# Kernel optimization log

Hardware: AMD Instinct MI355X
Metric: run time of the kernel (lower is better)

The kernel has to match this reference:

```python
import jax, jax.numpy as jnp
import numpy as np

B, L, D, CH, H = 16384, 50, 20, 16, 6


def setup_inputs() -> dict:
    key = jax.random.key(0)
    ks = jax.random.split(key, 18)
    s = 0.1
    return {
        "x": jax.random.normal(ks[0], (B, L, D), jnp.float32),
        "we_w": jax.random.normal(ks[1], (CH, D), jnp.float32) * s,
        "we_b": jax.random.normal(ks[2], (CH,), jnp.float32) * s,
        "attn_w": jax.random.normal(ks[3], (CH, CH), jnp.float32) * s,
        "attn_b": jax.random.normal(ks[4], (CH,), jnp.float32) * s,
        "conv1_w": jax.random.normal(ks[5], (CH, CH, 1), jnp.float32) * s,
        "conv1_b": jax.random.normal(ks[6], (CH,), jnp.float32) * s,
        "conv2_w": jax.random.normal(ks[7], (CH, CH, 3), jnp.float32) * s,
        "conv2_b": jax.random.normal(ks[8], (CH,), jnp.float32) * s,
        "conv3_w": jax.random.normal(ks[9], (CH, CH, 5), jnp.float32) * s,
        "conv3_b": jax.random.normal(ks[10], (CH,), jnp.float32) * s,
        "gru_wih": jax.random.normal(ks[11], (3 * H, CH), jnp.float32) * s,
        "gru_whh": jax.random.normal(ks[12], (3 * H, H), jnp.float32) * s,
        "gru_bih": jax.random.normal(ks[13], (3 * H,), jnp.float32) * s,
        "gru_bhh": jax.random.normal(ks[14], (3 * H,), jnp.float32) * s,
        "fc3_w": jax.random.normal(ks[15], (2, 3 * CH + H), jnp.float32) * s,
        "fc3_b": jax.random.normal(ks[16], (2,), jnp.float32) * s,
        "batchsize": B,
    }


def _conv1d(x, w, b, pad):
    # x: [B, C, L], w: [O, I, K] -> [B, O, L]
    y = jax.lax.conv_general_dilated(x, w, (1,), [(pad, pad)],
                                     dimension_numbers=("NCH", "OIH", "NCH"))
    return y + b[None, :, None]


def _gru(xg, wih, whh, bih, bhh):
    # xg: [B, L, CH] -> outputs [B, L, H] (PyTorch GRU equations, h0=0)
    gi = jnp.einsum("blc,gc->blg", xg, wih) + bih  # [B, L, 3H]
    gi_t = jnp.swapaxes(gi, 0, 1)                  # [L, B, 3H]
    h0 = jnp.zeros((xg.shape[0], H), xg.dtype)

    def step(h, gi_step):
        gh = h @ whh.T + bhh
        i_r, i_z, i_n = jnp.split(gi_step, 3, axis=-1)
        h_r, h_z, h_n = jnp.split(gh, 3, axis=-1)
        r = jax.nn.sigmoid(i_r + h_r)
        z = jax.nn.sigmoid(i_z + h_z)
        n = jnp.tanh(i_n + r * h_n)
        h_new = (1.0 - z) * n + z * h
        return h_new, h_new

    _, outs = jax.lax.scan(step, h0, gi_t)
    return jnp.swapaxes(outs, 0, 1)  # [B, L, H]


def reference(x, we_w, we_b, attn_w, attn_b, conv1_w, conv1_b, conv2_w, conv2_b,
              conv3_w, conv3_b, gru_wih, gru_whh, gru_bih, gru_bhh, fc3_w, fc3_b,
              batchsize):
    b = batchsize
    xe = x @ we_w.T + we_b                 # [B, L, CH]
    xr = xe.reshape(b, CH, L)              # RESHAPE (not transpose), as in torch

    lrelu = lambda v: jnp.where(v > 0, v, 0.1 * v)
    x1 = lrelu(_conv1d(xr, conv1_w, conv1_b, 0))
    x2 = lrelu(_conv1d(xr, conv2_w, conv2_b, 1))
    x3 = lrelu(_conv1d(xr, conv3_w, conv3_b, 2))

    xg = xr.reshape(b, L, CH)              # == xe
    x4 = _gru(xg, gru_wih, gru_whh, gru_bih, gru_bhh)  # [B, L, H]

    # dotproduct1: note x4.reshape([B,H,L]) is a reshape, NOT a transpose
    scores = jnp.matmul(x4, x4.reshape(b, H, L)) / H   # [B, L, L]
    alphas = jax.nn.softmax(scores, axis=1)            # softmax over dim=1 as in torch
    y = jnp.matmul(alphas, x4).reshape(b, H, L)        # [B, H, L]
    x_gru = jnp.sum(y, axis=2)                         # [B, H]

    # vectorized per-timestep attention loop: x[:, :, i] over i -> swapaxes
    xt = jnp.swapaxes(xr, 1, 2)                        # [B, L, CH]
    attn = jnp.tanh(xt @ attn_w.T + attn_b)            # [B, L, CH]
    attn1 = jnp.concatenate([attn, attn, attn], axis=2).reshape(b, 3 * CH, L)

    x_cat = jnp.concatenate([x1, x2, x3], axis=1)      # [B, 3CH, L]
    x_cnn = jnp.sum(x_cat * attn1, axis=2)             # [B, 3CH]

    feat = jnp.concatenate([x_cnn, x_gru], axis=1)     # [B, 3CH+H]
    return feat @ fc3_w.T + fc3_b                      # [B, 2]
```

## Files before the change

kernel.cpp:

```cpp
#include <hip/hip_runtime.h>

#define BATCH 16384
#define LSEQ  50
#define DIN   20
#define CHN   16
#define HID   6

__device__ __forceinline__ float frcp(float x){ return __builtin_amdgcn_rcpf(x); }
__device__ __forceinline__ float fsig(float x){ return frcp(1.0f + __expf(-x)); }
__device__ __forceinline__ float ftanh(float x){ float t = __expf(2.0f*x); return (t - 1.0f) * frcp(t + 1.0f); }
__device__ __forceinline__ float lrelu(float v){ return v > 0.0f ? v : 0.1f*v; }

constexpr int SLAB = 2560;

__global__ __launch_bounds__(256, 4) void fused_kernel(
    const float* __restrict__ x,
    const float* __restrict__ we_w, const float* __restrict__ we_b,
    const float* __restrict__ attn_w, const float* __restrict__ attn_b,
    const float* __restrict__ c1w, const float* __restrict__ c1b,
    const float* __restrict__ c2w, const float* __restrict__ c2b,
    const float* __restrict__ c3w, const float* __restrict__ c3b,
    const float* __restrict__ wih, const float* __restrict__ whh,
    const float* __restrict__ bih, const float* __restrict__ bhh,
    const float* __restrict__ fc3w, const float* __restrict__ fc3b,
    float* __restrict__ out)
{
  __shared__ __align__(16) float smem[4 * SLAB];
  const int tid  = threadIdx.x;
  const int wave = tid >> 6;
  const int lane = tid & 63;
  const int b    = blockIdx.x * 4 + wave;

  float* S    = smem + wave * SLAB;
  float* sXE  = S;
  float* sY   = S + 400;
  float* R1   = S + 800;
  float* sX4  = S + 1800;
  float* sX4P = S + 2104;
  float* sFE  = S + 2504;

  const float* xb = x + (size_t)b * (LSEQ * DIN);

  if (lane < LSEQ) {
    float xv[DIN];
    const float4* xr = (const float4*)(xb + lane * DIN);
    #pragma unroll
    for (int q = 0; q < 5; ++q) {
      float4 v = xr[q];
      xv[4*q] = v.x; xv[4*q+1] = v.y; xv[4*q+2] = v.z; xv[4*q+3] = v.w;
    }
    float xe[CHN];
    #pragma unroll
    for (int c = 0; c < CHN; ++c) {
      float a = we_b[c];
      #pragma unroll
      for (int d = 0; d < DIN; ++d) a = fmaf(xv[d], we_w[c * DIN + d], a);
      xe[c] = a;
    }
    float4* xd = (float4*)(sXE + lane * CHN);
    xd[0] = make_float4(xe[0], xe[1], xe[2], xe[3]);
    xd[1] = make_float4(xe[4], xe[5], xe[6], xe[7]);
    xd[2] = make_float4(xe[8], xe[9], xe[10], xe[11]);
    xd[3] = make_float4(xe[12], xe[13], xe[14], xe[15]);
    float gi[18];
    #pragma unroll
    for (int g = 0; g < 18; ++g) {
      float a = bih[g];
      #pragma unroll
      for (int cc = 0; cc < CHN; ++cc) a = fmaf(xe[cc], wih[g * CHN + cc], a);
      gi[g] = a;
    }
    float4* gd = (float4*)(R1 + lane * 20);
    gd[0] = make_float4(gi[0], gi[1], gi[2], gi[3]);
    gd[1] = make_float4(gi[4], gi[5], gi[6], gi[7]);
    gd[2] = make_float4(gi[8], gi[9], gi[10], gi[11]);
    gd[3] = make_float4(gi[12], gi[13], gi[14], gi[15]);
    *(float2*)(R1 + lane * 20 + 16) = make_float2(gi[16], gi[17]);
  }
  __syncthreads();

  {
    const int g18 = (lane < 18) ? lane : 0;
    float wh[HID];
    #pragma unroll
    for (int k = 0; k < HID; ++k) wh[k] = whh[g18 * HID + k];
    const float bh = bhh[g18];
    const int m6 = lane % 6;
    float hh[HID];
    #pragma unroll
    for (int k = 0; k < HID; ++k) hh[k] = 0.0f;
    float hm = 0.0f;
    for (int l = 0; l < LSEQ; ++l) {
      float gh = bh;
      #pragma unroll
      for (int k = 0; k < HID; ++k) gh = fmaf(wh[k], hh[k], gh);
      float ghr = __shfl(gh, m6);
      float ghz = __shfl(gh, m6 + 6);
      float ghn = __shfl(gh, m6 + 12);
      const float* gl = R1 + l * 20;
      float r  = fsig(gl[m6] + ghr);
      float z  = fsig(gl[m6 + 6] + ghz);
      float n  = ftanh(gl[m6 + 12] + r * ghn);
      float hn = fmaf(z, hm - n, n);
      hm = hn;
      #pragma unroll
      for (int k = 0; k < HID; ++k) hh[k] = __shfl(hn, k);
      if (lane < HID) { sX4[l * HID + lane] = hn; sX4P[l * 8 + lane] = hn; }
    }
  }
  __syncthreads();

  if (lane < LSEQ) {
    float a[CHN];
    #pragma unroll
    for (int cc = 0; cc < CHN; ++cc) a[cc] = sXE[cc * LSEQ + lane];
    float o[CHN];
    #pragma unroll
    for (int c = 0; c < CHN; ++c) {
      float acc = attn_b[c];
      #pragma unroll
      for (int cc = 0; cc < CHN; ++cc) acc = fmaf(a[cc], attn_w[c * CHN + cc], acc);
      o[c] = ftanh(acc);
    }
    float4* ad = (float4*)(R1 + lane * CHN);
    ad[0] = make_float4(o[0], o[1], o[2], o[3]);
    ad[1] = make_float4(o[4], o[5], o[6], o[7]);
    ad[2] = make_float4(o[8], o[9], o[10], o[11]);
    ad[3] = make_float4(o[12], o[13], o[14], o[15]);
  }
  __syncthreads();

  {
    float* sAT = R1;
    const int o = lane & 15;
    const int seg = lane >> 4;
    const int L0 = (seg < 2) ? seg * 13 : 26 + (seg - 2) * 12;
    const int NL = (seg < 2) ? 13 : 12;
    int mcl[17];
    #pragma unroll
    for (int mm = 0; mm < 17; ++mm) {
      int m = L0 - 2 + mm;
      mcl[mm] = min(max(m, 0), LSEQ - 1);
    }
    float z1[13], z2[13], z3[13];
    #pragma unroll
    for (int u = 0; u < 13; ++u) { z1[u] = 0.0f; z2[u] = 0.0f; z3[u] = 0.0f; }
    for (int i = 0; i < CHN; ++i) {
      const float w1 = c1w[o * CHN + i];
      float w2a[3], w3a[5];
      #pragma unroll
      for (int t = 0; t < 3; ++t) w2a[t] = c2w[(o * CHN + i) * 3 + t];
      #pragma unroll
      for (int t = 0; t < 5; ++t) w3a[t] = c3w[(o * CHN + i) * 5 + t];
      const float* xrow = sXE + i * LSEQ;
      float xv[17];
      #pragma unroll
      for (int mm = 0; mm < 17; ++mm) {
        float v = xrow[mcl[mm]];
        if (mm < 2 || mm >= 14) {
          int m = L0 - 2 + mm;
          v = (m == mcl[mm]) ? v : 0.0f;
        }
        xv[mm] = v;
      }
      #pragma unroll
      for (int u = 0; u < 13; ++u) {
        z1[u] = fmaf(w1, xv[u + 2], z1[u]);
        z2[u] = fmaf(w2a[0], xv[u + 1], z2[u]);
        z2[u] = fmaf(w2a[1], xv[u + 2], z2[u]);
        z2[u] = fmaf(w2a[2], xv[u + 3], z2[u]);
        z3[u] = fmaf(w3a[0], xv[u],     z3[u]);
        z3[u] = fmaf(w3a[1], xv[u + 1], z3[u]);
        z3[u] = fmaf(w3a[2], xv[u + 2], z3[u]);
        z3[u] = fmaf(w3a[3], xv[u + 3], z3[u]);
        z3[u] = fmaf(w3a[4], xv[u + 4], z3[u]);
      }
    }
    const float b1v = c1b[o], b2v = c2b[o], b3v = c3b[o];
    float a1 = 0.0f, a2 = 0.0f, a3 = 0.0f;
    #pragma unroll
    for (int u = 0; u < 13; ++u) {
      if (u < NL) {
        int l = L0 + u;
        float v1 = lrelu(z1[u] + b1v);
        float v2 = lrelu(z2[u] + b2v);
        float v3 = lrelu(z3[u] + b3v);
        int f1 = o * LSEQ + l;
        int f2 = (CHN + o) * LSEQ + l;
        int f3 = (2 * CHN + o) * LSEQ + l;
        a1 += v1 * sAT[(f1 / 48) * CHN + ((f1 % 48) & 15)];
        a2 += v2 * sAT[(f2 / 48) * CHN + ((f2 % 48) & 15)];
        a3 += v3 * sAT[(f3 / 48) * CHN + ((f3 % 48) & 15)];
      }
    }
    a1 += __shfl_xor(a1, 16); a1 += __shfl_xor(a1, 32);
    a2 += __shfl_xor(a2, 16); a2 += __shfl_xor(a2, 32);
    a3 += __shfl_xor(a3, 16); a3 += __shfl_xor(a3, 32);
    if (lane < CHN) { sFE[o] = a1; sFE[CHN + o] = a2; sFE[2 * CHN + o] = a3; }
  }
  __syncthreads();

  float* sC = R1;
  if (lane < LSEQ) {
    float colj[HID];
    #pragma unroll
    for (int h = 0; h < HID; ++h) colj[h] = sX4[h * LSEQ + lane];
    *(float4*)(sC + lane * 16)     = make_float4(colj[0], colj[1], colj[2], colj[3]);
    *(float2*)(sC + lane * 16 + 4) = make_float2(colj[4], colj[5]);
    float zs = 0.0f;
    for (int i = 0; i < LSEQ; ++i) {
      const float4 r0 = *(const float4*)(sX4P + i * 8);
      const float2 r1 = *(const float2*)(sX4P + i * 8 + 4);
      float s = r0.x * colj[0];
      s = fmaf(r0.y, colj[1], s); s = fmaf(r0.z, colj[2], s);
      s = fmaf(r0.w, colj[3], s); s = fmaf(r1.x, colj[4], s);
      s = fmaf(r1.y, colj[5], s);
      zs += __expf(s * (1.0f / 6.0f));
    }
    const float zi = frcp(zs);
    const float4 q0 = *(const float4*)(sX4P + lane * 8);
    const float2 q1 = *(const float2*)(sX4P + lane * 8 + 4);
    *(float4*)(sC + lane * 16 + 8)  = make_float4(zi*q0.x, zi*q0.y, zi*q0.z, zi*q0.w);
    *(float2*)(sC + lane * 16 + 12) = make_float2(zi*q1.x, zi*q1.y);
  }
  __syncthreads();

  if (lane < LSEQ) {
    float rowi[HID];
    {
      const float4 q0 = *(const float4*)(sX4P + lane * 8);
      const float2 q1 = *(const float2*)(sX4P + lane * 8 + 4);
      rowi[0] = q0.x; rowi[1] = q0.y; rowi[2] = q0.z;
      rowi[3] = q0.w; rowi[4] = q1.x; rowi[5] = q1.y;
    }
    float ya[HID];
    #pragma unroll
    for (int h = 0; h < HID; ++h) ya[h] = 0.0f;
    for (int j = 0; j < LSEQ; ++j) {
      const float4 t0 = *(const float4*)(sC + j * 16);
      const float2 t1 = *(const float2*)(sC + j * 16 + 4);
      float s = rowi[0] * t0.x;
      s = fmaf(rowi[1], t0.y, s); s = fmaf(rowi[2], t0.z, s);
      s = fmaf(rowi[3], t0.w, s); s = fmaf(rowi[4], t1.x, s);
      s = fmaf(rowi[5], t1.y, s);
      const float e = __expf(s * (1.0f / 6.0f));
      const float4 w0 = *(const float4*)(sC + j * 16 + 8);
      const float2 w1 = *(const float2*)(sC + j * 16 + 12);
      ya[0] = fmaf(e, w0.x, ya[0]);
      ya[1] = fmaf(e, w0.y, ya[1]);
      ya[2] = fmaf(e, w0.z, ya[2]);
      ya[3] = fmaf(e, w0.w, ya[3]);
      ya[4] = fmaf(e, w1.x, ya[4]);
      ya[5] = fmaf(e, w1.y, ya[5]);
    }
    *(float2*)(sY + lane * 6)     = make_float2(ya[0], ya[1]);
    *(float2*)(sY + lane * 6 + 2) = make_float2(ya[2], ya[3]);
    *(float2*)(sY + lane * 6 + 4) = make_float2(ya[4], ya[5]);
  }
  __syncthreads();

  if (lane < HID) {
    float s = 0.0f;
    for (int m = 0; m < LSEQ; ++m) s += sY[lane * LSEQ + m];
    sFE[48 + lane] = s;
  }
  __syncthreads();

  if (lane < 2) {
    float acc = fc3b[lane];
    const float* wr = fc3w + lane * 54;
    #pragma unroll
    for (int k = 0; k < 54; ++k) acc = fmaf(wr[k], sFE[k], acc);
    out[(size_t)b * 2 + lane] = acc;
  }
}

extern "C" void kernel_launch(void* const* d_in, const int* in_sizes, int n_in,
                              void* d_out, int out_size, void* d_ws, size_t ws_size,
                              hipStream_t stream) {
  (void)in_sizes; (void)n_in; (void)d_ws; (void)ws_size; (void)out_size;
  fused_kernel<<<BATCH / 4, 256, 0, stream>>>(
      (const float*)d_in[0],
      (const float*)d_in[1],  (const float*)d_in[2],
      (const float*)d_in[3],  (const float*)d_in[4],
      (const float*)d_in[5],  (const float*)d_in[6],
      (const float*)d_in[7],  (const float*)d_in[8],
      (const float*)d_in[9],  (const float*)d_in[10],
      (const float*)d_in[11], (const float*)d_in[12],
      (const float*)d_in[13], (const float*)d_in[14],
      (const float*)d_in[15], (const float*)d_in[16],
      (float*)d_out);
}
```

Baseline: 309.8 us.

## Split fused kernel into embed, per-thread GRU, and tail kernels via workspace

Splits the single fused kernel into three launches. An embedding/input-gate kernel writes xe and gi to global workspace. A GRU kernel then runs one batch element per thread, removing the per-step cross-lane shuffles and the 18-of-64 lane utilisation of the old recurrence. A tail kernel reloads xe and x4 to do the attention, convolutions and dot-product attention. This costs extra global-memory traffic (about 137 MB written and read back) and two extra launches, and it falls back to the fused kernel when the workspace is too small.

```diff
diff --git a/kernel.cpp b/kernel.cpp
--- a/kernel.cpp
+++ b/kernel.cpp
@@ -11,8 +11,333 @@
 __device__ __forceinline__ float ftanh(float x){ float t = __expf(2.0f*x); return (t - 1.0f) * frcp(t + 1.0f); }
 __device__ __forceinline__ float lrelu(float v){ return v > 0.0f ? v : 0.1f*v; }
 
+__global__ __launch_bounds__(256) void k_embed(
+    const float* __restrict__ x,
+    const float* __restrict__ we_w, const float* __restrict__ we_b,
+    const float* __restrict__ wih,  const float* __restrict__ bih,
+    float* __restrict__ xeg, float* __restrict__ gig)
+{
+  const size_t r = (size_t)blockIdx.x * 256 + threadIdx.x;
+  float xv[DIN];
+  const float4* xr = (const float4*)(x + r * DIN);
+  #pragma unroll
+  for (int q = 0; q < 5; ++q) {
+    float4 v = xr[q];
+    xv[4*q] = v.x; xv[4*q+1] = v.y; xv[4*q+2] = v.z; xv[4*q+3] = v.w;
+  }
+  float xe[CHN];
+  #pragma unroll
+  for (int c = 0; c < CHN; ++c) {
+    float a = we_b[c];
+    #pragma unroll
+    for (int d = 0; d < DIN; ++d) a = fmaf(xv[d], we_w[c * DIN + d], a);
+    xe[c] = a;
+  }
+  float4* xo = (float4*)(xeg + r * CHN);
+  xo[0] = make_float4(xe[0],  xe[1],  xe[2],  xe[3]);
+  xo[1] = make_float4(xe[4],  xe[5],  xe[6],  xe[7]);
+  xo[2] = make_float4(xe[8],  xe[9],  xe[10], xe[11]);
+  xo[3] = make_float4(xe[12], xe[13], xe[14], xe[15]);
+  float gi[18];
+  #pragma unroll
+  for (int g = 0; g < 18; ++g) {
+    float a = bih[g];
+    #pragma unroll
+    for (int c = 0; c < CHN; ++c) a = fmaf(xe[c], wih[g * CHN + c], a);
+    gi[g] = a;
+  }
+  float* go = gig + r * 20;
+  ((float4*)go)[0] = make_float4(gi[0],  gi[1],  gi[2],  gi[3]);
+  ((float4*)go)[1] = make_float4(gi[4],  gi[5],  gi[6],  gi[7]);
+  ((float4*)go)[2] = make_float4(gi[8],  gi[9],  gi[10], gi[11]);
+  ((float4*)go)[3] = make_float4(gi[12], gi[13], gi[14], gi[15]);
+  *(float2*)(go + 16) = make_float2(gi[16], gi[17]);
+}
+
+__global__ __launch_bounds__(64) void k_gru(
+    const float* __restrict__ gig,
+    const float* __restrict__ whh, const float* __restrict__ bhh,
+    float* __restrict__ x4g)
+{
+  const int b = blockIdx.x * 64 + threadIdx.x;
+  float wh[18][HID];
+  #pragma unroll
+  for (int g = 0; g < 18; ++g)
+    #pragma unroll
+    for (int k = 0; k < HID; ++k) wh[g][k] = whh[g * HID + k];
+  float bh[18];
+  #pragma unroll
+  for (int g = 0; g < 18; ++g) bh[g] = bhh[g];
+
+  const float* gp = gig + (size_t)b * (LSEQ * 20);
+  float* op = x4g + (size_t)b * (LSEQ * HID);
+
+  float h[HID];
+  #pragma unroll
+  for (int k = 0; k < HID; ++k) h[k] = 0.0f;
+
+  float cur[18];
+  {
+    const float4* q = (const float4*)gp;
+    float4 a0 = q[0], a1 = q[1], a2 = q[2], a3 = q[3];
+    float2 a4 = *(const float2*)(gp + 16);
+    cur[0]=a0.x; cur[1]=a0.y; cur[2]=a0.z; cur[3]=a0.w;
+    cur[4]=a1.x; cur[5]=a1.y; cur[6]=a1.z; cur[7]=a1.w;
+    cur[8]=a2.x; cur[9]=a2.y; cur[10]=a2.z; cur[11]=a2.w;
+    cur[12]=a3.x; cur[13]=a3.y; cur[14]=a3.z; cur[15]=a3.w;
+    cur[16]=a4.x; cur[17]=a4.y;
+  }
+
+  for (int l = 0; l < LSEQ; ++l) {
+    float nxt[18];
+    if (l < LSEQ - 1) {
+      const float* np = gp + (l + 1) * 20;
+      const float4* q = (const float4*)np;
+      float4 a0 = q[0], a1 = q[1], a2 = q[2], a3 = q[3];
+      float2 a4 = *(const float2*)(np + 16);
+      nxt[0]=a0.x; nxt[1]=a0.y; nxt[2]=a0.z; nxt[3]=a0.w;
+      nxt[4]=a1.x; nxt[5]=a1.y; nxt[6]=a1.z; nxt[7]=a1.w;
+      nxt[8]=a2.x; nxt[9]=a2.y; nxt[10]=a2.z; nxt[11]=a2.w;
+      nxt[12]=a3.x; nxt[13]=a3.y; nxt[14]=a3.z; nxt[15]=a3.w;
+      nxt[16]=a4.x; nxt[17]=a4.y;
+    }
+    float gh[18];
+    #pragma unroll
+    for (int g = 0; g < 18; ++g) {
+      float a = bh[g];
+      #pragma unroll
+      for (int k = 0; k < HID; ++k) a = fmaf(wh[g][k], h[k], a);
+      gh[g] = a;
+    }
+    float r6[HID], z6[HID];
+    #pragma unroll
+    for (int m = 0; m < HID; ++m) r6[m] = fsig(cur[m] + gh[m]);
+    #pragma unroll
+    for (int m = 0; m < HID; ++m) z6[m] = fsig(cur[6 + m] + gh[6 + m]);
+    #pragma unroll
+    for (int m = 0; m < HID; ++m) {
+      float n = ftanh(fmaf(r6[m], gh[12 + m], cur[12 + m]));
+      h[m] = fmaf(z6[m], h[m] - n, n);
+    }
+    *(float2*)(op + l * HID)     = make_float2(h[0], h[1]);
+    *(float2*)(op + l * HID + 2) = make_float2(h[2], h[3]);
+    *(float2*)(op + l * HID + 4) = make_float2(h[4], h[5]);
+    #pragma unroll
+    for (int g = 0; g < 18; ++g) cur[g] = nxt[g];
+  }
+}
+
+constexpr int SLAB3 = 2368;
+
+__global__ __launch_bounds__(256, 4) void k_tail(
+    const float* __restrict__ xeg, const float* __restrict__ x4g,
+    const float* __restrict__ attn_w, const float* __restrict__ attn_b,
+    const float* __restrict__ c1w, const float* __restrict__ c1b,
+    const float* __restrict__ c2w, const float* __restrict__ c2b,
+    const float* __restrict__ c3w, const float* __restrict__ c3b,
+    const float* __restrict__ fc3w, const float* __restrict__ fc3b,
+    float* __restrict__ out)
+{
+  __shared__ __align__(16) float smem[4 * SLAB3];
+  const int tid  = threadIdx.x;
+  const int wave = tid >> 6;
+  const int lane = tid & 63;
+  const int b    = blockIdx.x * 4 + wave;
+
+  float* S    = smem + wave * SLAB3;
+  float* sXE  = S;
+  float* sY   = S + 400;
+  float* R1   = S + 800;
+  float* sX4  = S + 1600;
+  float* sX4P = S + 1904;
+  float* sFE  = S + 2304;
+
+  {
+    const float4* xs = (const float4*)(xeg + (size_t)b * 800);
+    float4* xd = (float4*)sXE;
+    #pragma unroll
+    for (int q = 0; q < 3; ++q) xd[lane + 64 * q] = xs[lane + 64 * q];
+    if (lane < 8) xd[lane + 192] = xs[lane + 192];
+    const float4* hs = (const float4*)(x4g + (size_t)b * 300);
+    float4* hd = (float4*)sX4;
+    hd[lane < 64 ? lane : 0] = hs[lane < 64 ? lane : 0];
+    if (lane < 11) hd[lane + 64] = hs[lane + 64];
+  }
+  __syncthreads();
+  if (lane < LSEQ) {
+    float2 a = *(float2*)(sX4 + lane * 6);
+    float2 c = *(float2*)(sX4 + lane * 6 + 2);
+    float2 d = *(float2*)(sX4 + lane * 6 + 4);
+    *(float2*)(sX4P + lane * 8)     = a;
+    *(float2*)(sX4P + lane * 8 + 2) = c;
+    *(float2*)(sX4P + lane * 8 + 4) = d;
+  }
+
+  if (lane < LSEQ) {
+    float a[CHN];
+    #pragma unroll
+    for (int cc = 0; cc < CHN; ++cc) a[cc] = sXE[cc * LSEQ + lane];
+    float o[CHN];
+    #pragma unroll
+    for (int c = 0; c < CHN; ++c) {
+      float acc = attn_b[c];
+      #pragma unroll
+      for (int cc = 0; cc < CHN; ++cc) acc = fmaf(a[cc], attn_w[c * CHN + cc], acc);
+      o[c] = ftanh(acc);
+    }
+    float4* ad = (float4*)(R1 + lane * CHN);
+    ad[0] = make_float4(o[0],  o[1],  o[2],  o[3]);
+    ad[1] = make_float4(o[4],  o[5],  o[6],  o[7]);
+    ad[2] = make_float4(o[8],  o[9],  o[10], o[11]);
+    ad[3] = make_float4(o[12], o[13], o[14], o[15]);
+  }
+  __syncthreads();
+
+  {
+    float* sAT = R1;
+    const int o = lane & 15;
+    const int seg = lane >> 4;
+    const int L0 = (seg < 2) ? seg * 13 : 26 + (seg - 2) * 12;
+    const int NL = (seg < 2) ? 13 : 12;
+    int mcl[17];
+    #pragma unroll
+    for (int mm = 0; mm < 17; ++mm) {
+      int m = L0 - 2 + mm;
+      mcl[mm] = min(max(m, 0), LSEQ - 1);
+    }
+    float z1[13], z2[13], z3[13];
+    #pragma unroll
+    for (int u = 0; u < 13; ++u) { z1[u] = 0.0f; z2[u] = 0.0f; z3[u] = 0.0f; }
+    for (int i = 0; i < CHN; ++i) {
+      const float w1 = c1w[o * CHN + i];
+      float w2a[3], w3a[5];
+      #pragma unroll
+      for (int t = 0; t < 3; ++t) w2a[t] = c2w[(o * CHN + i) * 3 + t];
+      #pragma unroll
+      for (int t = 0; t < 5; ++t) w3a[t] = c3w[(o * CHN + i) * 5 + t];
+      const float* xrow = sXE + i * LSEQ;
+      float xv[17];
+      #pragma unroll
+      for (int mm = 0; mm < 17; ++mm) {
+        float v = xrow[mcl[mm]];
+        if (mm < 2 || mm >= 14) {
+          int m = L0 - 2 + mm;
+          v = (m == mcl[mm]) ? v : 0.0f;
+        }
+        xv[mm] = v;
+      }
+      #pragma unroll
+      for (int u = 0; u < 13; ++u) {
+        z1[u] = fmaf(w1, xv[u + 2], z1[u]);
+        z2[u] = fmaf(w2a[0], xv[u + 1], z2[u]);
+        z2[u] = fmaf(w2a[1], xv[u + 2], z2[u]);
+        z2[u] = fmaf(w2a[2], xv[u + 3], z2[u]);
+        z3[u] = fmaf(w3a[0], xv[u],     z3[u]);
+        z3[u] = fmaf(w3a[1], xv[u + 1], z3[u]);
+        z3[u] = fmaf(w3a[2], xv[u + 2], z3[u]);
+        z3[u] = fmaf(w3a[3], xv[u + 3], z3[u]);
+        z3[u] = fmaf(w3a[4], xv[u + 4], z3[u]);
+      }
+    }
+    const float b1v = c1b[o], b2v = c2b[o], b3v = c3b[o];
+    float a1 = 0.0f, a2 = 0.0f, a3 = 0.0f;
+    #pragma unroll
+    for (int u = 0; u < 13; ++u) {
+      if (u < NL) {
+        int l = L0 + u;
+        float v1 = lrelu(z1[u] + b1v);
+        float v2 = lrelu(z2[u] + b2v);
+        float v3 = lrelu(z3[u] + b3v);
+        int f1 = o * LSEQ + l;
+        int f2 = (CHN + o) * LSEQ + l;
+        int f3 = (2 * CHN + o) * LSEQ + l;
+        a1 += v1 * sAT[(f1 / 48) * CHN + ((f1 % 48) & 15)];
+        a2 += v2 * sAT[(f2 / 48) * CHN + ((f2 % 48) & 15)];
+        a3 += v3 * sAT[(f3 / 48) * CHN + ((f3 % 48) & 15)];
+      }
+    }
+    a1 += __shfl_xor(a1, 16); a1 += __shfl_xor(a1, 32);
+    a2 += __shfl_xor(a2, 16); a2 += __shfl_xor(a2, 32);
+    a3 += __shfl_xor(a3, 16); a3 += __shfl_xor(a3, 32);
+    if (lane < CHN) { sFE[o] = a1; sFE[CHN + o] = a2; sFE[2 * CHN + o] = a3; }
+  }
+  __syncthreads();
+
+  float* sC = R1;
+  if (lane < LSEQ) {
+    float colj[HID];
+    #pragma unroll
+    for (int h = 0; h < HID; ++h) colj[h] = sX4[h * LSEQ + lane];
+    *(float4*)(sC + lane * 16)     = make_float4(colj[0], colj[1], colj[2], colj[3]);
+    *(float2*)(sC + lane * 16 + 4) = make_float2(colj[4], colj[5]);
+    float zs = 0.0f;
+    for (int i = 0; i < LSEQ; ++i) {
+      const float4 r0 = *(const float4*)(sX4P + i * 8);
+      const float2 r1 = *(const float2*)(sX4P + i * 8 + 4);
+      float s = r0.x * colj[0];
+      s = fmaf(r0.y, colj[1], s); s = fmaf(r0.z, colj[2], s);
+      s = fmaf(r0.w, colj[3], s); s = fmaf(r1.x, colj[4], s);
+      s = fmaf(r1.y, colj[5], s);
+      zs += __expf(s * (1.0f / 6.0f));
+    }
+    const float zi = frcp(zs);
+    const float4 q0 = *(const float4*)(sX4P + lane * 8);
+    const float2 q1 = *(const float2*)(sX4P + lane * 8 + 4);
+    *(float4*)(sC + lane * 16 + 8)  = make_float4(zi*q0.x, zi*q0.y, zi*q0.z, zi*q0.w);
+    *(float2*)(sC + lane * 16 + 12) = make_float2(zi*q1.x, zi*q1.y);
+  }
+  __syncthreads();
+
+  if (lane < LSEQ) {
+    float rowi[HID];
+    {
+      const float4 q0 = *(const float4*)(sX4P + lane * 8);
+      const float2 q1 = *(const float2*)(sX4P + lane * 8 + 4);
+      rowi[0] = q0.x; rowi[1] = q0.y; rowi[2] = q0.z;
+      rowi[3] = q0.w; rowi[4] = q1.x; rowi[5] = q1.y;
+    }
+    float ya[HID];
+    #pragma unroll
+    for (int h = 0; h < HID; ++h) ya[h] = 0.0f;
+    for (int j = 0; j < LSEQ; ++j) {
+      const float4 t0 = *(const float4*)(sC + j * 16);
+      const float2 t1 = *(const float2*)(sC + j * 16 + 4);
+      float s = rowi[0] * t0.x;
+      s = fmaf(rowi[1], t0.y, s); s = fmaf(rowi[2], t0.z, s);
+      s = fmaf(rowi[3], t0.w, s); s = fmaf(rowi[4], t1.x, s);
+      s = fmaf(rowi[5], t1.y, s);
+      const float e = __expf(s * (1.0f / 6.0f));
+      const float4 w0 = *(const float4*)(sC + j * 16 + 8);
+      const float2 w1 = *(const float2*)(sC + j * 16 + 12);
+      ya[0] = fmaf(e, w0.x, ya[0]);
+      ya[1] = fmaf(e, w0.y, ya[1]);
+      ya[2] = fmaf(e, w0.z, ya[2]);
+      ya[3] = fmaf(e, w0.w, ya[3]);
+      ya[4] = fmaf(e, w1.x, ya[4]);
+      ya[5] = fmaf(e, w1.y, ya[5]);
+    }
+    *(float2*)(sY + lane * 6)     = make_float2(ya[0], ya[1]);
+    *(float2*)(sY + lane * 6 + 2) = make_float2(ya[2], ya[3]);
+    *(float2*)(sY + lane * 6 + 4) = make_float2(ya[4], ya[5]);
+  }
+  __syncthreads();
+
+  if (lane < HID) {
+    float s = 0.0f;
+    for (int m = 0; m < LSEQ; ++m) s += sY[lane * LSEQ + m];
+    sFE[48 + lane] = s;
+  }
+  __syncthreads();
+  if (lane < 2) {
+    float acc = fc3b[lane];
+    const float* wr = fc3w + lane * 54;
+    #pragma unroll
+    for (int k = 0; k < 54; ++k) acc = fmaf(wr[k], sFE[k], acc);
+    out[(size_t)b * 2 + lane] = acc;
+  }
+}
+
 constexpr int SLAB = 2560;
-
 __global__ __launch_bounds__(256, 4) void fused_kernel(
     const float* __restrict__ x,
     const float* __restrict__ we_w, const float* __restrict__ we_b,
@@ -30,7 +355,6 @@
   const int wave = tid >> 6;
   const int lane = tid & 63;
   const int b    = blockIdx.x * 4 + wave;
-
   float* S    = smem + wave * SLAB;
   float* sXE  = S;
   float* sY   = S + 400;
@@ -38,17 +362,12 @@
   float* sX4  = S + 1800;
   float* sX4P = S + 2104;
   float* sFE  = S + 2504;
-
   const float* xb = x + (size_t)b * (LSEQ * DIN);
-
   if (lane < LSEQ) {
     float xv[DIN];
     const float4* xr = (const float4*)(xb + lane * DIN);
     #pragma unroll
-    for (int q = 0; q < 5; ++q) {
-      float4 v = xr[q];
-      xv[4*q] = v.x; xv[4*q+1] = v.y; xv[4*q+2] = v.z; xv[4*q+3] = v.w;
-    }
+    for (int q = 0; q < 5; ++q) { float4 v = xr[q]; xv[4*q]=v.x; xv[4*q+1]=v.y; xv[4*q+2]=v.z; xv[4*q+3]=v.w; }
     float xe[CHN];
     #pragma unroll
     for (int c = 0; c < CHN; ++c) {
@@ -78,7 +397,6 @@
     *(float2*)(R1 + lane * 20 + 16) = make_float2(gi[16], gi[17]);
   }
   __syncthreads();
-
   {
     const int g18 = (lane < 18) ? lane : 0;
     float wh[HID];
@@ -109,7 +427,6 @@
     }
   }
   __syncthreads();
-
   if (lane < LSEQ) {
     float a[CHN];
     #pragma unroll
@@ -129,7 +446,6 @@
     ad[3] = make_float4(o[12], o[13], o[14], o[15]);
   }
   __syncthreads();
-
   {
     float* sAT = R1;
     const int o = lane & 15;
@@ -138,10 +454,7 @@
     const int NL = (seg < 2) ? 13 : 12;
     int mcl[17];
     #pragma unroll
-    for (int mm = 0; mm < 17; ++mm) {
-      int m = L0 - 2 + mm;
-      mcl[mm] = min(max(m, 0), LSEQ - 1);
-    }
+    for (int mm = 0; mm < 17; ++mm) { int m = L0 - 2 + mm; mcl[mm] = min(max(m, 0), LSEQ - 1); }
     float z1[13], z2[13], z3[13];
     #pragma unroll
     for (int u = 0; u < 13; ++u) { z1[u] = 0.0f; z2[u] = 0.0f; z3[u] = 0.0f; }
@@ -157,10 +470,7 @@
       #pragma unroll
       for (int mm = 0; mm < 17; ++mm) {
         float v = xrow[mcl[mm]];
-        if (mm < 2 || mm >= 14) {
-          int m = L0 - 2 + mm;
-          v = (m == mcl[mm]) ? v : 0.0f;
-        }
+        if (mm < 2 || mm >= 14) { int m = L0 - 2 + mm; v = (m == mcl[mm]) ? v : 0.0f; }
         xv[mm] = v;
       }
       #pragma unroll
@@ -199,7 +509,6 @@
     if (lane < CHN) { sFE[o] = a1; sFE[CHN + o] = a2; sFE[2 * CHN + o] = a3; }
   }
   __syncthreads();
-
   float* sC = R1;
   if (lane < LSEQ) {
     float colj[HID];
@@ -224,7 +533,6 @@
     *(float2*)(sC + lane * 16 + 12) = make_float2(zi*q1.x, zi*q1.y);
   }
   __syncthreads();
-
   if (lane < LSEQ) {
     float rowi[HID];
     {
@@ -258,14 +566,12 @@
     *(float2*)(sY + lane * 6 + 4) = make_float2(ya[4], ya[5]);
   }
   __syncthreads();
-
   if (lane < HID) {
     float s = 0.0f;
     for (int m = 0; m < LSEQ; ++m) s += sY[lane * LSEQ + m];
     sFE[48 + lane] = s;
   }
   __syncthreads();
-
   if (lane < 2) {
     float acc = fc3b[lane];
     const float* wr = fc3w + lane * 54;
@@ -278,16 +584,43 @@
 extern "C" void kernel_launch(void* const* d_in, const int* in_sizes, int n_in,
                               void* d_out, int out_size, void* d_ws, size_t ws_size,
                               hipStream_t stream) {
-  (void)in_sizes; (void)n_in; (void)d_ws; (void)ws_size; (void)out_size;
-  fused_kernel<<<BATCH / 4, 256, 0, stream>>>(
-      (const float*)d_in[0],
-      (const float*)d_in[1],  (const float*)d_in[2],
-      (const float*)d_in[3],  (const float*)d_in[4],
-      (const float*)d_in[5],  (const float*)d_in[6],
-      (const float*)d_in[7],  (const float*)d_in[8],
-      (const float*)d_in[9],  (const float*)d_in[10],
-      (const float*)d_in[11], (const float*)d_in[12],
-      (const float*)d_in[13], (const float*)d_in[14],
-      (const float*)d_in[15], (const float*)d_in[16],
-      (float*)d_out);
+  (void)in_sizes; (void)n_in; (void)out_size;
+  const float* x      = (const float*)d_in[0];
+  const float* we_w   = (const float*)d_in[1];
+  const float* we_b   = (const float*)d_in[2];
+  const float* attn_w = (const float*)d_in[3];
+  const float* attn_b = (const float*)d_in[4];
+  const float* c1w    = (const float*)d_in[5];
+  const float* c1b    = (const float*)d_in[6];
+  const float* c2w    = (const float*)d_in[7];
+  const float* c2b    = (const float*)d_in[8];
+  const float* c3w    = (const float*)d_in[9];
+  const float* c3b    = (const float*)d_in[10];
+  const float* wih    = (const float*)d_in[11];
+  const float* whh    = (const float*)d_in[12];
+  const float* bih    = (const float*)d_in[13];
+  const float* bhh    = (const float*)d_in[14];
+  const float* fc3w   = (const float*)d_in[15];
+  const float* fc3b   = (const float*)d_in[16];
+  float* out = (float*)d_out;
+
+  const size_t xe_elems = (size_t)BATCH * 800;
+  const size_t gi_elems = (size_t)BATCH * 1000;
+  const size_t x4_elems = (size_t)BATCH * 300;
+  const size_t need = (xe_elems + gi_elems + x4_elems) * sizeof(float);
+
+  if (ws_size >= need) {
+    float* xeg = (float*)d_ws;
+    float* gig = xeg + xe_elems;
+    float* x4g = gig + gi_elems;
+    k_embed<<<(BATCH * LSEQ) / 256, 256, 0, stream>>>(x, we_w, we_b, wih, bih, xeg, gig);
+    k_gru<<<BATCH / 64, 64, 0, stream>>>(gig, whh, bhh, x4g);
+    k_tail<<<BATCH / 4, 256, 0, stream>>>(xeg, x4g, attn_w, attn_b,
+                                          c1w, c1b, c2w, c2b, c3w, c3b,
+                                          fc3w, fc3b, out);
+  } else {
+    fused_kernel<<<BATCH / 4, 256, 0, stream>>>(
+        x, we_w, we_b, attn_w, attn_b, c1w, c1b, c2w, c2b, c3w, c3b,
+        wih, whh, bih, bhh, fc3w, fc3b, out);
+  }
 }
```

Result: slower. 346.0 us (+11.7%).

## Pack four samples' GRU recurrences into one wave using 16-lane groups

Applied to the files above, without the earlier changes.

The GRU recurrence, previously run redundantly-wide by every wave with one sample each, now runs only in wave 0, which handles all four samples of the block in 16-lane groups. Each lane computes two hidden-gate dot products, and the r/z/n gate values are exchanged through shuffles within the group. This frees the other three waves' issue slots during the serial 50-step loop so co-resident blocks can use the SIMDs. The cost is that those waves sit idle at the barrier, and the per-step dependency chain in wave 0 may get slightly longer.

```diff
diff --git a/kernel.cpp b/kernel.cpp
--- a/kernel.cpp
+++ b/kernel.cpp
@@ -79,33 +79,51 @@
   }
   __syncthreads();
 
-  {
-    const int g18 = (lane < 18) ? lane : 0;
-    float wh[HID];
-    #pragma unroll
-    for (int k = 0; k < HID; ++k) wh[k] = whh[g18 * HID + k];
-    const float bh = bhh[g18];
-    const int m6 = lane % 6;
+  if (wave == 0) {
+    const int q = lane >> 4;
+    const int g = lane & 15;
+    const int gb = 16 + (g & 1);
+    float wa[HID], wb[HID];
+    #pragma unroll
+    for (int k = 0; k < HID; ++k) { wa[k] = whh[g * HID + k]; wb[k] = whh[gb * HID + k]; }
+    const float ba = bhh[g];
+    const float bb = bhh[gb];
+
+    float* giq  = smem + q * SLAB + 800;
+    float* x4q  = smem + q * SLAB + 1800;
+    float* x4pq = smem + q * SLAB + 2104;
+
+    const int base   = q << 4;
+    const int srcZ   = base + 6 + g;
+    const int srcN   = base + ((g < 4) ? (12 + g) : (g - 4));
+
     float hh[HID];
     #pragma unroll
     for (int k = 0; k < HID; ++k) hh[k] = 0.0f;
-    float hm = 0.0f;
+
     for (int l = 0; l < LSEQ; ++l) {
-      float gh = bh;
-      #pragma unroll
-      for (int k = 0; k < HID; ++k) gh = fmaf(wh[k], hh[k], gh);
-      float ghr = __shfl(gh, m6);
-      float ghz = __shfl(gh, m6 + 6);
-      float ghn = __shfl(gh, m6 + 12);
-      const float* gl = R1 + l * 20;
-      float r  = fsig(gl[m6] + ghr);
-      float z  = fsig(gl[m6 + 6] + ghz);
-      float n  = ftanh(gl[m6 + 12] + r * ghn);
-      float hn = fmaf(z, hm - n, n);
-      hm = hn;
-      #pragma unroll
-      for (int k = 0; k < HID; ++k) hh[k] = __shfl(hn, k);
-      if (lane < HID) { sX4[l * HID + lane] = hn; sX4P[l * 8 + lane] = hn; }
+      const float gia = giq[l * 20 + g];
+      const float gib = giq[l * 20 + gb];
+      float gha = ba, ghb = bb;
+      #pragma unroll
+      for (int k = 0; k < HID; ++k) {
+        gha = fmaf(wa[k], hh[k], gha);
+        ghb = fmaf(wb[k], hh[k], ghb);
+      }
+      const float siga = fsig(gia + gha);
+      const float ghx = (g >= 12) ? gha : ghb;
+      const float gix = (g >= 12) ? gia : gib;
+      const float ghn = __shfl(ghx, srcN);
+      const float gin = __shfl(gix, srcN);
+      const float z   = __shfl(siga, srcZ);
+      const float n   = ftanh(fmaf(siga, ghn, gin));
+      const float hn  = fmaf(z, hh[g < HID ? g : 0] - n, n);
+      if (g < HID) {
+        x4q[l * HID + g] = hn;
+        x4pq[l * 8 + g]  = hn;
+      }
+      #pragma unroll
+      for (int k = 0; k < HID; ++k) hh[k] = __shfl(hn, base + k);
     }
   }
   __syncthreads();
```

After: 294.5 us. -5.0%, faster.
